# Kernel tuning notes

Hardware: AMD Instinct MI355X
Metric: run time of the kernel (lower is better)

Reference implementation:

```python
import jax, jax.numpy as jnp
import numpy as np

IN_FRAC = 11
OUT_FRAC = 10

def _make_luts():
    seg_fp = jnp.linspace(-8.0, 6.0, 17)
    silu_fp = seg_fp * jax.nn.sigmoid(seg_fp)
    # torch stores these as int16; values fit easily, we keep int32 for arithmetic
    seg = jnp.round(seg_fp * (1 << IN_FRAC)).astype(jnp.int32)
    silu_vals = jnp.round(silu_fp * (1 << OUT_FRAC)).astype(jnp.int32)
    return seg, silu_vals

def setup_inputs() -> dict:
    key = jax.random.key(0)
    x = jax.random.normal(key, (8, 2048, 4096), dtype=jnp.float32)
    seg, silu_vals = _make_luts()
    return {"x": x, "seg": seg, "silu_vals": silu_vals}

def reference(x, seg, silu_vals):
    x_int = jnp.round(x * (1 << IN_FRAC)).astype(jnp.int32)
    min_seg = seg[0]
    max_seg = seg[-1]
    # right branch: x_int > max_seg -> simple rescale shift (in_frac - out_frac = 1)
    mask_right = x_int > max_seg
    right_val = x_int >> (IN_FRAC - OUT_FRAC)
    # piecewise-linear interpolation branch
    x_clamped = jnp.clip(x_int, min_seg, max_seg)
    # torch.bucketize(right=False) == searchsorted side='left'
    idx = jnp.clip(jnp.searchsorted(seg, x_clamped, side='left') - 1, 0, seg.shape[0] - 2)
    x0 = seg[idx]
    x1 = seg[idx + 1]
    y0 = silu_vals[idx]
    y1 = silu_vals[idx + 1]
    dx = x_clamped - x0                      # >= 0
    dx_total = jnp.maximum(x1 - x0, 1)       # eps clamp
    t_fx = ((dx << OUT_FRAC) + dx_total // 2) // dx_total
    dy = y1 - y0
    # precedence as in torch source: (t_fx*dy + (1 << (out_frac-1))) >> out_frac
    interp = y0 + ((t_fx * dy + (1 << (OUT_FRAC - 1))) >> OUT_FRAC)
    out_int = jnp.where(mask_right, right_val, interp)
    return out_int.astype(jnp.float32) / (1 << OUT_FRAC)
```

## Files before the change

### kernel.cpp

```cpp
#include <hip/hip_runtime.h>

#define MIN_SEG  (-16384)
#define MAX_SEG  (12288)
#define D_SEG    (1792)

__global__ __launch_bounds__(256)
void approx_silu_fxp_kernel(const float* __restrict__ x,
                            const int* __restrict__ silu_vals,
                            float* __restrict__ out,
                            int n4) {
    __shared__ int lut[17];
    if (threadIdx.x < 17) lut[threadIdx.x] = silu_vals[threadIdx.x];
    __syncthreads();

    const float4* __restrict__ x4 = reinterpret_cast<const float4*>(x);
    float4* __restrict__ o4 = reinterpret_cast<float4*>(out);

    int stride = gridDim.x * blockDim.x;
    for (int i = blockIdx.x * blockDim.x + threadIdx.x; i < n4; i += stride) {
        float4 v = x4[i];
        float r[4] = {v.x, v.y, v.z, v.w};
        float o[4];
        #pragma unroll
        for (int j = 0; j < 4; ++j) {
            int xi = __float2int_rn(r[j] * 2048.0f);
            int out_int;
            if (xi > MAX_SEG) {
                out_int = xi >> 1;
            } else {
                int xc = max(xi, MIN_SEG);
                unsigned u = (unsigned)(xc - MIN_SEG);
                int idx = min((int)(u / D_SEG), 15);
                int dx  = (int)u - idx * D_SEG;
                int y0 = lut[idx];
                int y1 = lut[idx + 1];
                int t_fx = (dx * 1024 + 896) / D_SEG;
                out_int = y0 + ((t_fx * (y1 - y0) + 512) >> 10);
            }
            o[j] = (float)out_int * (1.0f / 1024.0f);
        }
        float4 ov = make_float4(o[0], o[1], o[2], o[3]);
        o4[i] = ov;
    }
}

extern "C" void kernel_launch(void* const* d_in, const int* in_sizes, int n_in,
                              void* d_out, int out_size, void* d_ws, size_t ws_size,
                              hipStream_t stream) {
    const float* x = (const float*)d_in[0];
    const int* silu_vals = (const int*)d_in[2];
    float* out = (float*)d_out;

    int n = in_sizes[0];
    int n4 = n >> 2;

    int block = 256;
    int grid = (n4 + block - 1) / block;
    if (grid > 2048) grid = 2048;

    approx_silu_fxp_kernel<<<grid, block, 0, stream>>>(x, silu_vals, out, n4);
}
```

Before: 103.6 us.

## Use nontemporal vector loads/stores and unroll grid-stride loop by four

Replaces the plain float4 loads and stores with nontemporal builtins so streaming data skips normal cache retention. The grid-stride loop is unrolled four ways with all four loads issued before any compute, giving more bytes in flight per thread. The fixed-point division now uses unsigned constants, which lets the compiler emit a cheaper magic-multiply sequence. The grid is fixed at 2048 blocks, and a remainder loop handles the tail.

```diff
diff --git a/kernel.cpp b/kernel.cpp
--- a/kernel.cpp
+++ b/kernel.cpp
@@ -4,43 +4,68 @@
 #define MAX_SEG  (12288)
 #define D_SEG    (1792)
 
+typedef float f32x4 __attribute__((ext_vector_type(4)));
+
+__device__ __forceinline__ float silu_one(float xf, const int* __restrict__ lut) {
+    int xi = __float2int_rn(xf * 2048.0f);
+    int out_int;
+    if (xi > MAX_SEG) {
+        out_int = xi >> 1;
+    } else {
+        int xc = max(xi, MIN_SEG);
+        unsigned u = (unsigned)(xc - MIN_SEG);
+        int idx = min((int)(u / D_SEG), 15);
+        int dx  = (int)u - idx * D_SEG;
+        int y0 = lut[idx];
+        int y1 = lut[idx + 1];
+        int t_fx = (int)((dx * 1024u + 896u) / 1792u);
+        out_int = y0 + ((t_fx * (y1 - y0) + 512) >> 10);
+    }
+    return (float)out_int * (1.0f / 1024.0f);
+}
+
 __global__ __launch_bounds__(256)
-void approx_silu_fxp_kernel(const float* __restrict__ x,
-                            const int* __restrict__ silu_vals,
-                            float* __restrict__ out,
-                            int n4) {
+void approx_silu_fxp_nt_kernel(const float* __restrict__ x,
+                               const int* __restrict__ silu_vals,
+                               float* __restrict__ out,
+                               int n4) {
     __shared__ int lut[17];
     if (threadIdx.x < 17) lut[threadIdx.x] = silu_vals[threadIdx.x];
     __syncthreads();
 
-    const float4* __restrict__ x4 = reinterpret_cast<const float4*>(x);
-    float4* __restrict__ o4 = reinterpret_cast<float4*>(out);
+    const f32x4* __restrict__ xv = reinterpret_cast<const f32x4*>(x);
+    f32x4* __restrict__ ov = reinterpret_cast<f32x4*>(out);
 
-    int stride = gridDim.x * blockDim.x;
-    for (int i = blockIdx.x * blockDim.x + threadIdx.x; i < n4; i += stride) {
-        float4 v = x4[i];
-        float r[4] = {v.x, v.y, v.z, v.w};
-        float o[4];
+    const int stride = gridDim.x * blockDim.x;
+    int i = blockIdx.x * blockDim.x + threadIdx.x;
+
+    for (; i + 3 * stride < n4; i += 4 * stride) {
+        f32x4 v0 = __builtin_nontemporal_load(xv + i);
+        f32x4 v1 = __builtin_nontemporal_load(xv + i + stride);
+        f32x4 v2 = __builtin_nontemporal_load(xv + i + 2 * stride);
+        f32x4 v3 = __builtin_nontemporal_load(xv + i + 3 * stride);
+
+        f32x4 o0, o1, o2, o3;
         #pragma unroll
-        for (int j = 0; j < 4; ++j) {
-            int xi = __float2int_rn(r[j] * 2048.0f);
-            int out_int;
-            if (xi > MAX_SEG) {
-                out_int = xi >> 1;
-            } else {
-                int xc = max(xi, MIN_SEG);
-                unsigned u = (unsigned)(xc - MIN_SEG);
-                int idx = min((int)(u / D_SEG), 15);
-                int dx  = (int)u - idx * D_SEG;
-                int y0 = lut[idx];
-                int y1 = lut[idx + 1];
-                int t_fx = (dx * 1024 + 896) / D_SEG;
-                out_int = y0 + ((t_fx * (y1 - y0) + 512) >> 10);
-            }
-            o[j] = (float)out_int * (1.0f / 1024.0f);
-        }
-        float4 ov = make_float4(o[0], o[1], o[2], o[3]);
-        o4[i] = ov;
+        for (int j = 0; j < 4; ++j) o0[j] = silu_one(v0[j], lut);
+        #pragma unroll
+        for (int j = 0; j < 4; ++j) o1[j] = silu_one(v1[j], lut);
+        #pragma unroll
+        for (int j = 0; j < 4; ++j) o2[j] = silu_one(v2[j], lut);
+        #pragma unroll
+        for (int j = 0; j < 4; ++j) o3[j] = silu_one(v3[j], lut);
+
+        __builtin_nontemporal_store(o0, ov + i);
+        __builtin_nontemporal_store(o1, ov + i + stride);
+        __builtin_nontemporal_store(o2, ov + i + 2 * stride);
+        __builtin_nontemporal_store(o3, ov + i + 3 * stride);
+    }
+    for (; i < n4; i += stride) {
+        f32x4 v = __builtin_nontemporal_load(xv + i);
+        f32x4 o;
+        #pragma unroll
+        for (int j = 0; j < 4; ++j) o[j] = silu_one(v[j], lut);
+        __builtin_nontemporal_store(o, ov + i);
     }
 }
 
@@ -55,8 +80,6 @@
     int n4 = n >> 2;
 
     int block = 256;
-    int grid = (n4 + block - 1) / block;
-    if (grid > 2048) grid = 2048;
-
-    approx_silu_fxp_kernel<<<grid, block, 0, stream>>>(x, silu_vals, out, n4);
+    int grid = 2048;
+    approx_silu_fxp_nt_kernel<<<grid, block, 0, stream>>>(x, silu_vals, out, n4);
 }
```

Result: slower. 112.5 us (+8.6%).
